# Kernel tuning notes

Measured on AMD Instinct MI355X. Metric: run time of the kernel, lower is better.

The kernel has to match this reference:

```python
import jax, jax.numpy as jnp
import numpy as np

NEG_BIG = -9.0e15  # matches torch zero_vec constant


def setup_inputs() -> dict:
    key = jax.random.key(0)
    k1, k2, k3, k4, k5 = jax.random.split(key, 5)
    B, N, D_IN, D_HID, D_OUT = 4, 4096, 128, 64, 128
    h = jax.random.normal(k1, (B, N, D_IN), dtype=jnp.float32)
    adj = jax.random.randint(k2, (N, N), 0, 2, dtype=jnp.int32)
    Ws = jax.random.normal(k3, (D_IN, D_HID), dtype=jnp.float32) * (1.414 / np.sqrt(D_IN))
    Wt = jax.random.normal(k4, (D_IN, D_HID), dtype=jnp.float32) * (1.414 / np.sqrt(D_IN))
    Wc = jax.random.normal(k5, (D_IN, D_OUT), dtype=jnp.float32) * np.sqrt(2.0 / D_IN)
    return {"h": h, "adj": adj, "Ws": Ws, "Wt": Wt, "Wc": Wc}


def reference(h, adj, Ws, Wt, Wc):
    # h: [B,N,D_in], adj: [N,N] broadcast over batch
    Whs = jnp.matmul(h, Ws)                     # [B,N,H]
    Wht = jnp.matmul(h, Wt)                     # [B,N,H]
    e = jnp.einsum('bnh,bmh->bnm', Whs, Wht)    # [B,N,N] dense scores
    z = jnp.where(adj > 0, e, NEG_BIG)          # adjacency mask
    alpha = jax.nn.softmax(z, axis=-1)          # [B,N,N]
    Whc = jnp.matmul(h, Wc)                     # [B,N,D_out]
    h_prime = jnp.matmul(alpha, Whc)            # [B,N,D_out]
    return h_prime
```

## Files before the change

kernel.cpp:

```cpp
#include <hip/hip_runtime.h>
#include <hip/hip_bf16.h>

#define NTOK 4096
#define BATCH 4
#define DIN 128
#define DHID 64
#define DOUT 128
#define NWRD (NTOK / 32)
#define NEG_BIG -9.0e15f
#define LOG2E 1.44269504088896340736f

typedef short short8 __attribute__((ext_vector_type(8)));
typedef float floatx4 __attribute__((ext_vector_type(4)));

static __device__ __forceinline__ unsigned short f2bf(float f) {
    unsigned int u = __builtin_bit_cast(unsigned int, f);
    u = (u + 0x7fffu + ((u >> 16) & 1u)) >> 16;
    return (unsigned short)u;
}
static __device__ __forceinline__ float bf2f(unsigned short s) {
    unsigned int u = ((unsigned int)s) << 16;
    return __builtin_bit_cast(float, u);
}
static __device__ __forceinline__ unsigned int pk2(float lo, float hi) {
    unsigned int r;
    asm("v_cvt_pk_bf16_f32 %0, %1, %2" : "=v"(r) : "v"(lo), "v"(hi));
    return r;
}

static __device__ __forceinline__ floatx4 mfma16(short8 a, short8 b, floatx4 c) {
    return __builtin_amdgcn_mfma_f32_16x16x32_bf16(a, b, c, 0, 0, 0);
}

__global__ __launch_bounds__(256) void pack_adj_kernel(const int* __restrict__ adj,
                                                       unsigned int* __restrict__ bits) {
    int w = blockIdx.x * 256 + threadIdx.x;
    const int4* p = reinterpret_cast<const int4*>(adj) + (size_t)w * 8;
    unsigned int m = 0;
#pragma unroll
    for (int i = 0; i < 8; ++i) {
        int4 v = p[i];
        m |= (v.x > 0 ? 1u : 0u) << (4 * i + 0);
        m |= (v.y > 0 ? 1u : 0u) << (4 * i + 1);
        m |= (v.z > 0 ? 1u : 0u) << (4 * i + 2);
        m |= (v.w > 0 ? 1u : 0u) << (4 * i + 3);
    }
    bits[w] = m;
}

__global__ __launch_bounds__(256) void conv_w_kernel(const float* __restrict__ Ws,
                                                     const float* __restrict__ Wt,
                                                     const float* __restrict__ Wc,
                                                     unsigned short* __restrict__ WT_hi,
                                                     unsigned short* __restrict__ WT_lo) {
    int idx = blockIdx.x * 256 + threadIdx.x;
    int k = idx >> 8, col = idx & 255;
    float w;
    if (col < 64) w = Ws[k * DHID + col] * LOG2E;
    else if (col < 128) w = Wt[k * DHID + (col - 64)];
    else w = Wc[k * DOUT + (col - 128)];
    unsigned short hi = f2bf(w);
    WT_hi[col * DIN + k] = hi;
    if (col < 128) WT_lo[col * DIN + k] = f2bf(w - bf2f(hi));
}

__global__ __launch_bounds__(256) void prep_kernel(const float* __restrict__ h,
                                                   const unsigned short* __restrict__ WT_hi,
                                                   const unsigned short* __restrict__ WT_lo,
                                                   unsigned short* __restrict__ Whs_hi,
                                                   unsigned short* __restrict__ Whs_lo,
                                                   unsigned short* __restrict__ Wht_hi,
                                                   unsigned short* __restrict__ Wht_lo,
                                                   unsigned short* __restrict__ WhcT) {
    int tid = threadIdx.x;
    int b = blockIdx.y;
    int w = tid >> 6, lane = tid & 63, lg = lane >> 4, lc = lane & 15;
    int n0 = blockIdx.x * 16;
    const float* hrow = h + (size_t)(b * NTOK + n0 + lc) * DIN;

    short8 ah[4], al[4];
#pragma unroll
    for (int ks = 0; ks < 4; ++ks) {
        float4 f0 = *reinterpret_cast<const float4*>(hrow + ks * 32 + lg * 8);
        float4 f1 = *reinterpret_cast<const float4*>(hrow + ks * 32 + lg * 8 + 4);
        float x[8] = {f0.x, f0.y, f0.z, f0.w, f1.x, f1.y, f1.z, f1.w};
        short8 hh, ll;
#pragma unroll
        for (int j = 0; j < 8; ++j) {
            unsigned short hb = f2bf(x[j]);
            hh[j] = (short)hb;
            ll[j] = (short)f2bf(x[j] - bf2f(hb));
        }
        ah[ks] = hh;
        al[ks] = ll;
    }

#pragma unroll
    for (int ci = 0; ci < 4; ++ci) {
        int ct = w * 4 + ci;
        int col = ct * 16 + lc;
        const unsigned short* bbase = WT_hi + (size_t)col * DIN;
        const unsigned short* lbase = WT_lo + (size_t)col * DIN;
        floatx4 acc = {0.f, 0.f, 0.f, 0.f};
#pragma unroll
        for (int ks = 0; ks < 4; ++ks) {
            short8 bh = *reinterpret_cast<const short8*>(bbase + ks * 32 + lg * 8);
            acc = mfma16(ah[ks], bh, acc);
            if (w < 2) {
                short8 bl = *reinterpret_cast<const short8*>(lbase + ks * 32 + lg * 8);
                acc = mfma16(ah[ks], bl, acc);
                acc = mfma16(al[ks], bh, acc);
            }
        }
        int nr = n0 + 4 * lg;
        if (w == 0) {
#pragma unroll
            for (int r = 0; r < 4; ++r) {
                float v = acc[r];
                unsigned short hb = f2bf(v);
                size_t o = (size_t)(b * NTOK + nr + r) * DHID + col;
                Whs_hi[o] = hb;
                Whs_lo[o] = f2bf(v - bf2f(hb));
            }
        } else if (w == 1) {
#pragma unroll
            for (int r = 0; r < 4; ++r) {
                float v = acc[r];
                unsigned short hb = f2bf(v);
                size_t o = (size_t)(b * NTOK + nr + r) * DHID + (col - 64);
                Wht_hi[o] = hb;
                Wht_lo[o] = f2bf(v - bf2f(hb));
            }
        } else {
            unsigned int p01 = (unsigned int)f2bf(acc[0]) | ((unsigned int)f2bf(acc[1]) << 16);
            unsigned int p23 = (unsigned int)f2bf(acc[2]) | ((unsigned int)f2bf(acc[3]) << 16);
            unsigned int* dst =
                reinterpret_cast<unsigned int*>(&WhcT[(size_t)(b * DOUT + col - 128) * NTOK + nr]);
            dst[0] = p01;
            dst[1] = p23;
        }
    }
}

template <int ITERS>
__global__ __launch_bounds__(256, 2) void attn_kernel(const unsigned short* __restrict__ Whs_hi,
                                                      const unsigned short* __restrict__ Whs_lo,
                                                      const unsigned short* __restrict__ Wht_hi,
                                                      const unsigned short* __restrict__ Wht_lo,
                                                      const unsigned short* __restrict__ WhcT,
                                                      const unsigned int* __restrict__ bits,
                                                      unsigned short* __restrict__ po,
                                                      float* __restrict__ pm,
                                                      float* __restrict__ pl) {
    __shared__ unsigned short Kh_lds[64][72];
    __shared__ unsigned short Kl_lds[64][72];
    __shared__ unsigned short V_lds[128][72];

    int tid = threadIdx.x;
    int b = blockIdx.y;
    int split = blockIdx.z;
    int kbase = split * (ITERS * 64);
    int lane = tid & 63, lg = lane >> 4, lc = lane & 15;
    int q0 = blockIdx.x * 128 + (tid >> 6) * 32;
    int nA = q0 + lc, nB = q0 + 16 + lc;

    const unsigned short* qAH = Whs_hi + (size_t)(b * NTOK + nA) * DHID;
    const unsigned short* qAL = Whs_lo + (size_t)(b * NTOK + nA) * DHID;
    const unsigned short* qBH = Whs_hi + (size_t)(b * NTOK + nB) * DHID;
    const unsigned short* qBL = Whs_lo + (size_t)(b * NTOK + nB) * DHID;
    short8 qAh0 = *reinterpret_cast<const short8*>(qAH + lg * 8);
    short8 qAh1 = *reinterpret_cast<const short8*>(qAH + 32 + lg * 8);
    short8 qAl0 = *reinterpret_cast<const short8*>(qAL + lg * 8);
    short8 qAl1 = *reinterpret_cast<const short8*>(qAL + 32 + lg * 8);
    short8 qBh0 = *reinterpret_cast<const short8*>(qBH + lg * 8);
    short8 qBh1 = *reinterpret_cast<const short8*>(qBH + 32 + lg * 8);
    short8 qBl0 = *reinterpret_cast<const short8*>(qBL + lg * 8);
    short8 qBl1 = *reinterpret_cast<const short8*>(qBL + 32 + lg * 8);

    floatx4 o0[8], o1[8];
#pragma unroll
    for (int dt = 0; dt < 8; ++dt) {
        o0[dt] = (floatx4){0.f, 0.f, 0.f, 0.f};
        o1[dt] = (floatx4){0.f, 0.f, 0.f, 0.f};
    }
    float mA = NEG_BIG, lA = 0.f, mB = NEG_BIG, lB = 0.f;

    int kkey = tid >> 2, koff = (tid & 3) * 16;
    int vd = tid >> 1, va = tid & 1;

    short8 krH0, krH1, krL0, krL1, vr0, vr1, vr2, vr3;
    unsigned int mwA0, mwA1, mwB0, mwB1;

    {
        int kb = kbase;
        const unsigned short* ksrcH = Wht_hi + (size_t)(b * NTOK + kb + kkey) * DHID + koff;
        const unsigned short* ksrcL = Wht_lo + (size_t)(b * NTOK + kb + kkey) * DHID + koff;
        krH0 = *reinterpret_cast<const short8*>(ksrcH);
        krH1 = *reinterpret_cast<const short8*>(ksrcH + 8);
        krL0 = *reinterpret_cast<const short8*>(ksrcL);
        krL1 = *reinterpret_cast<const short8*>(ksrcL + 8);
        const unsigned short* vsrc = WhcT + (size_t)(b * DOUT + vd) * NTOK + kb + va * 32;
        vr0 = *reinterpret_cast<const short8*>(vsrc);
        vr1 = *reinterpret_cast<const short8*>(vsrc + 8);
        vr2 = *reinterpret_cast<const short8*>(vsrc + 16);
        vr3 = *reinterpret_cast<const short8*>(vsrc + 24);
        mwA0 = bits[nA * NWRD + (kb >> 5)];
        mwA1 = bits[nA * NWRD + (kb >> 5) + 1];
        mwB0 = bits[nB * NWRD + (kb >> 5)];
        mwB1 = bits[nB * NWRD + (kb >> 5) + 1];
    }

    for (int it = 0; it < ITERS; ++it) {
        __syncthreads();
        *reinterpret_cast<short8*>(&Kh_lds[kkey][koff]) = krH0;
        *reinterpret_cast<short8*>(&Kh_lds[kkey][koff + 8]) = krH1;
        *reinterpret_cast<short8*>(&Kl_lds[kkey][koff]) = krL0;
        *reinterpret_cast<short8*>(&Kl_lds[kkey][koff + 8]) = krL1;
        {
            int sb = va * 32;
            short8 w00 = __builtin_shufflevector(vr0, vr2, 0, 1, 2, 3, 8, 9, 10, 11);
            short8 w01 = __builtin_shufflevector(vr0, vr2, 4, 5, 6, 7, 12, 13, 14, 15);
            short8 w10 = __builtin_shufflevector(vr1, vr3, 0, 1, 2, 3, 8, 9, 10, 11);
            short8 w11 = __builtin_shufflevector(vr1, vr3, 4, 5, 6, 7, 12, 13, 14, 15);
            *reinterpret_cast<short8*>(&V_lds[vd][sb]) = w00;
            *reinterpret_cast<short8*>(&V_lds[vd][sb + 8]) = w01;
            *reinterpret_cast<short8*>(&V_lds[vd][sb + 16]) = w10;
            *reinterpret_cast<short8*>(&V_lds[vd][sb + 24]) = w11;
        }
        __syncthreads();

        floatx4 s0[4], s1[4];
        __builtin_amdgcn_s_setprio(1);
#pragma unroll
        for (int kc = 0; kc < 4; ++kc) {
            short8 kh0 = *reinterpret_cast<const short8*>(&Kh_lds[kc * 16 + lc][lg * 8]);
            short8 kh1 = *reinterpret_cast<const short8*>(&Kh_lds[kc * 16 + lc][32 + lg * 8]);
            short8 kl0 = *reinterpret_cast<const short8*>(&Kl_lds[kc * 16 + lc][lg * 8]);
            short8 kl1 = *reinterpret_cast<const short8*>(&Kl_lds[kc * 16 + lc][32 + lg * 8]);
            floatx4 a0 = {0.f, 0.f, 0.f, 0.f};
            a0 = mfma16(kh0, qAh0, a0);
            a0 = mfma16(kh1, qAh1, a0);
            a0 = mfma16(kh0, qAl0, a0);
            a0 = mfma16(kh1, qAl1, a0);
            a0 = mfma16(kl0, qAh0, a0);
            a0 = mfma16(kl1, qAh1, a0);
            s0[kc] = a0;
            floatx4 a1 = {0.f, 0.f, 0.f, 0.f};
            a1 = mfma16(kh0, qBh0, a1);
            a1 = mfma16(kh1, qBh1, a1);
            a1 = mfma16(kh0, qBl0, a1);
            a1 = mfma16(kh1, qBl1, a1);
            a1 = mfma16(kl0, qBh0, a1);
            a1 = mfma16(kl1, qBh1, a1);
            s1[kc] = a1;
        }
        __builtin_amdgcn_s_setprio(0);

#pragma unroll
        for (int kc = 0; kc < 4; ++kc) {
            unsigned int wA = (kc & 2) ? mwA1 : mwA0;
            unsigned int wB = (kc & 2) ? mwB1 : mwB0;
#pragma unroll
            for (int r = 0; r < 4; ++r) {
                int bit = 16 * (kc & 1) + 4 * lg + r;
                if (!((wA >> bit) & 1u)) s0[kc][r] = NEG_BIG;
                if (!((wB >> bit) & 1u)) s1[kc][r] = NEG_BIG;
            }
        }

        if (it + 1 < ITERS) {
            int kb = kbase + (it + 1) * 64;
            const unsigned short* ksrcH = Wht_hi + (size_t)(b * NTOK + kb + kkey) * DHID + koff;
            const unsigned short* ksrcL = Wht_lo + (size_t)(b * NTOK + kb + kkey) * DHID + koff;
            krH0 = *reinterpret_cast<const short8*>(ksrcH);
            krH1 = *reinterpret_cast<const short8*>(ksrcH + 8);
            krL0 = *reinterpret_cast<const short8*>(ksrcL);
            krL1 = *reinterpret_cast<const short8*>(ksrcL + 8);
            const unsigned short* vsrc = WhcT + (size_t)(b * DOUT + vd) * NTOK + kb + va * 32;
            vr0 = *reinterpret_cast<const short8*>(vsrc);
            vr1 = *reinterpret_cast<const short8*>(vsrc + 8);
            vr2 = *reinterpret_cast<const short8*>(vsrc + 16);
            vr3 = *reinterpret_cast<const short8*>(vsrc + 24);
            mwA0 = bits[nA * NWRD + (kb >> 5)];
            mwA1 = bits[nA * NWRD + (kb >> 5) + 1];
            mwB0 = bits[nB * NWRD + (kb >> 5)];
            mwB1 = bits[nB * NWRD + (kb >> 5) + 1];
        }

        {
            float vm = s0[0][0];
#pragma unroll
            for (int kc = 0; kc < 4; ++kc)
#pragma unroll
                for (int r = 0; r < 4; ++r) vm = fmaxf(vm, s0[kc][r]);
            vm = fmaxf(vm, __shfl_xor(vm, 16));
            vm = fmaxf(vm, __shfl_xor(vm, 32));
            bool skip = __all(vm <= mA + 4.0f);
            float mn = skip ? mA : fmaxf(mA, vm);
            float rs = 0.f;
#pragma unroll
            for (int kc = 0; kc < 4; ++kc)
#pragma unroll
                for (int r = 0; r < 4; ++r) {
                    float p = exp2f(s0[kc][r] - mn);
                    s0[kc][r] = p;
                    rs += p;
                }
            rs += __shfl_xor(rs, 16);
            rs += __shfl_xor(rs, 32);
            if (!skip) {
                float sc = exp2f(mA - mn);
                lA = lA * sc + rs;
                mA = mn;
                float sc4[4];
#pragma unroll
                for (int r = 0; r < 4; ++r) sc4[r] = __shfl(sc, (lane & 48) + 4 * lg + r);
#pragma unroll
                for (int dt = 0; dt < 8; ++dt)
#pragma unroll
                    for (int r = 0; r < 4; ++r) o0[dt][r] *= sc4[r];
            } else {
                lA += rs;
            }
        }
        {
            float vm = s1[0][0];
#pragma unroll
            for (int kc = 0; kc < 4; ++kc)
#pragma unroll
                for (int r = 0; r < 4; ++r) vm = fmaxf(vm, s1[kc][r]);
            vm = fmaxf(vm, __shfl_xor(vm, 16));
            vm = fmaxf(vm, __shfl_xor(vm, 32));
            bool skip = __all(vm <= mB + 4.0f);
            float mn = skip ? mB : fmaxf(mB, vm);
            float rs = 0.f;
#pragma unroll
            for (int kc = 0; kc < 4; ++kc)
#pragma unroll
                for (int r = 0; r < 4; ++r) {
                    float p = exp2f(s1[kc][r] - mn);
                    s1[kc][r] = p;
                    rs += p;
                }
            rs += __shfl_xor(rs, 16);
            rs += __shfl_xor(rs, 32);
            if (!skip) {
                float sc = exp2f(mB - mn);
                lB = lB * sc + rs;
                mB = mn;
                float sc4[4];
#pragma unroll
                for (int r = 0; r < 4; ++r) sc4[r] = __shfl(sc, (lane & 48) + 4 * lg + r);
#pragma unroll
                for (int dt = 0; dt < 8; ++dt)
#pragma unroll
                    for (int r = 0; r < 4; ++r) o1[dt][r] *= sc4[r];
            } else {
                lB += rs;
            }
        }

        unsigned int pw[8];
        pw[0] = pk2(s0[0][0], s0[0][1]); pw[1] = pk2(s0[0][2], s0[0][3]);
        pw[2] = pk2(s0[1][0], s0[1][1]); pw[3] = pk2(s0[1][2], s0[1][3]);
        pw[4] = pk2(s0[2][0], s0[2][1]); pw[5] = pk2(s0[2][2], s0[2][3]);
        pw[6] = pk2(s0[3][0], s0[3][1]); pw[7] = pk2(s0[3][2], s0[3][3]);
        short8 paA0 = __builtin_bit_cast(short8, *reinterpret_cast<uint4*>(&pw[0]));
        short8 paA1 = __builtin_bit_cast(short8, *reinterpret_cast<uint4*>(&pw[4]));
        pw[0] = pk2(s1[0][0], s1[0][1]); pw[1] = pk2(s1[0][2], s1[0][3]);
        pw[2] = pk2(s1[1][0], s1[1][1]); pw[3] = pk2(s1[1][2], s1[1][3]);
        pw[4] = pk2(s1[2][0], s1[2][1]); pw[5] = pk2(s1[2][2], s1[2][3]);
        pw[6] = pk2(s1[3][0], s1[3][1]); pw[7] = pk2(s1[3][2], s1[3][3]);
        short8 paB0 = __builtin_bit_cast(short8, *reinterpret_cast<uint4*>(&pw[0]));
        short8 paB1 = __builtin_bit_cast(short8, *reinterpret_cast<uint4*>(&pw[4]));

        __builtin_amdgcn_s_setprio(1);
#pragma unroll
        for (int dt = 0; dt < 8; ++dt) {
            short8 vf0 = *reinterpret_cast<const short8*>(&V_lds[dt * 16 + lc][lg * 8]);
            o0[dt] = mfma16(paA0, vf0, o0[dt]);
            o1[dt] = mfma16(paB0, vf0, o1[dt]);
        }
#pragma unroll
        for (int dt = 0; dt < 8; ++dt) {
            short8 vf1 = *reinterpret_cast<const short8*>(&V_lds[dt * 16 + lc][32 + lg * 8]);
            o0[dt] = mfma16(paA1, vf1, o0[dt]);
            o1[dt] = mfma16(paB1, vf1, o1[dt]);
        }
        __builtin_amdgcn_s_setprio(0);
    }

    {
        float m4[4], l4[4];
#pragma unroll
        for (int r = 0; r < 4; ++r) {
            int src = (lane & 48) + 4 * lg + r;
            m4[r] = __shfl(mA, src);
            l4[r] = __shfl(lA, src);
        }
#pragma unroll
        for (int r = 0; r < 4; ++r) {
            size_t row = (size_t)(split * BATCH + b) * NTOK + q0 + 4 * lg + r;
            unsigned short* prow = po + row * DOUT;
#pragma unroll
            for (int dt = 0; dt < 8; ++dt) prow[dt * 16 + lc] = f2bf(o0[dt][r]);
            if (lc == 0) {
                pm[row] = m4[r];
                pl[row] = l4[r];
            }
        }
#pragma unroll
        for (int r = 0; r < 4; ++r) {
            int src = (lane & 48) + 4 * lg + r;
            m4[r] = __shfl(mB, src);
            l4[r] = __shfl(lB, src);
        }
#pragma unroll
        for (int r = 0; r < 4; ++r) {
            size_t row = (size_t)(split * BATCH + b) * NTOK + q0 + 16 + 4 * lg + r;
            unsigned short* prow = po + row * DOUT;
#pragma unroll
            for (int dt = 0; dt < 8; ++dt) prow[dt * 16 + lc] = f2bf(o1[dt][r]);
            if (lc == 0) {
                pm[row] = m4[r];
                pl[row] = l4[r];
            }
        }
    }
}

template <int NSPLIT>
__global__ __launch_bounds__(256) void merge_kernel(const unsigned short* __restrict__ po,
                                                    const float* __restrict__ pm,
                                                    const float* __restrict__ pl,
                                                    float* __restrict__ out) {
    int idx = blockIdx.x * 256 + threadIdx.x;
    int d = idx & (DOUT - 1);
    size_t bn = (size_t)(idx >> 7);
    const size_t BN = (size_t)BATCH * NTOK;

    float ms[NSPLIT];
#pragma unroll
    for (int s = 0; s < NSPLIT; ++s) ms[s] = pm[s * BN + bn];
    float M = ms[0];
#pragma unroll
    for (int s = 1; s < NSPLIT; ++s) M = fmaxf(M, ms[s]);
    float L = 0.f, acc = 0.f;
#pragma unroll
    for (int s = 0; s < NSPLIT; ++s) {
        float e = exp2f(ms[s] - M);
        L += pl[s * BN + bn] * e;
        acc += bf2f(po[(s * BN + bn) * DOUT + d]) * e;
    }
    out[idx] = acc / L;
}

extern "C" void kernel_launch(void* const* d_in, const int* in_sizes, int n_in,
                              void* d_out, int out_size, void* d_ws, size_t ws_size,
                              hipStream_t stream) {
    const float* h   = (const float*)d_in[0];
    const int*   adj = (const int*)d_in[1];
    const float* Ws  = (const float*)d_in[2];
    const float* Wt  = (const float*)d_in[3];
    const float* Wc  = (const float*)d_in[4];
    float* out = (float*)d_out;

    size_t nq = (size_t)BATCH * NTOK * DHID;
    unsigned short* Whs_hi = (unsigned short*)d_ws;
    unsigned short* Whs_lo = Whs_hi + nq;
    unsigned short* Wht_hi = Whs_lo + nq;
    unsigned short* Wht_lo = Wht_hi + nq;
    unsigned short* WhcT   = Wht_lo + nq;
    unsigned int*   bits   = (unsigned int*)(WhcT + (size_t)BATCH * DOUT * NTOK);
    unsigned short* WT_hi  = (unsigned short*)(bits + (size_t)NTOK * NWRD);
    unsigned short* WT_lo  = WT_hi + 256 * DIN;
    unsigned short* po     = WT_lo + 128 * DIN;
    const size_t BASE = (size_t)((char*)po - (char*)d_ws);

    size_t need8 = BASE + 8 * ((size_t)BATCH * NTOK * DOUT * 2 + (size_t)BATCH * NTOK * 8);
    int use8 = (ws_size >= need8) ? 1 : 0;
    int nsplit = use8 ? 8 : 4;

    float* pm = (float*)(po + (size_t)nsplit * BATCH * NTOK * DOUT);
    float* pl = pm + (size_t)nsplit * BATCH * NTOK;

    pack_adj_kernel<<<dim3(NTOK * NWRD / 256), dim3(256), 0, stream>>>(adj, bits);
    conv_w_kernel<<<dim3(128), dim3(256), 0, stream>>>(Ws, Wt, Wc, WT_hi, WT_lo);
    prep_kernel<<<dim3(NTOK / 16, BATCH), dim3(256), 0, stream>>>(
        h, WT_hi, WT_lo, Whs_hi, Whs_lo, Wht_hi, Wht_lo, WhcT);
    if (use8) {
        attn_kernel<8><<<dim3(NTOK / 128, BATCH, 8), dim3(256), 0, stream>>>(
            Whs_hi, Whs_lo, Wht_hi, Wht_lo, WhcT, bits, po, pm, pl);
        merge_kernel<8><<<dim3(BATCH * NTOK * DOUT / 256), dim3(256), 0, stream>>>(po, pm, pl, out);
    } else {
        attn_kernel<16><<<dim3(NTOK / 128, BATCH, 4), dim3(256), 0, stream>>>(
            Whs_hi, Whs_lo, Wht_hi, Wht_lo, WhcT, bits, po, pm, pl);
        merge_kernel<4><<<dim3(BATCH * NTOK * DOUT / 256), dim3(256), 0, stream>>>(po, pm, pl, out);
    }
}
```

Before: 200.0 us.

## Double-buffer K/V tiles in LDS, pre-permute V layout, fix split to 4

The attention kernel now keeps two LDS buffers for the K (hi/lo) and V tiles. The next tile is written to the idle buffer after compute, and global loads are issued two iterations ahead, which removes one barrier per iteration. The V shuffle is moved into the prep kernel by storing WhcT in a pre-permuted column order, so the kernel writes registers straight to LDS. The split count is fixed at 4 instead of picking 8 when workspace allows. LDS use doubles, which may limit occupancy, and fewer splits give fewer blocks.

```diff
diff --git a/kernel.cpp b/kernel.cpp
--- a/kernel.cpp
+++ b/kernel.cpp
@@ -7,6 +7,8 @@
 #define DHID 64
 #define DOUT 128
 #define NWRD (NTOK / 32)
+#define SPLIT 4
+#define ITERS (NTOK / SPLIT / 64)
 #define NEG_BIG -9.0e15f
 #define LOG2E 1.44269504088896340736f
 
@@ -132,17 +134,17 @@
                 Wht_lo[o] = f2bf(v - bf2f(hb));
             }
         } else {
+            int pcol = (nr & ~31) | ((nr & 8) << 1) | ((nr & 4) << 1) | ((nr & 16) >> 2);
             unsigned int p01 = (unsigned int)f2bf(acc[0]) | ((unsigned int)f2bf(acc[1]) << 16);
             unsigned int p23 = (unsigned int)f2bf(acc[2]) | ((unsigned int)f2bf(acc[3]) << 16);
             unsigned int* dst =
-                reinterpret_cast<unsigned int*>(&WhcT[(size_t)(b * DOUT + col - 128) * NTOK + nr]);
+                reinterpret_cast<unsigned int*>(&WhcT[(size_t)(b * DOUT + col - 128) * NTOK + pcol]);
             dst[0] = p01;
             dst[1] = p23;
         }
     }
 }
 
-template <int ITERS>
 __global__ __launch_bounds__(256, 2) void attn_kernel(const unsigned short* __restrict__ Whs_hi,
                                                       const unsigned short* __restrict__ Whs_lo,
                                                       const unsigned short* __restrict__ Wht_hi,
@@ -152,9 +154,9 @@
                                                       unsigned short* __restrict__ po,
                                                       float* __restrict__ pm,
                                                       float* __restrict__ pl) {
-    __shared__ unsigned short Kh_lds[64][72];
-    __shared__ unsigned short Kl_lds[64][72];
-    __shared__ unsigned short V_lds[128][72];
+    __shared__ unsigned short Kh_lds[2][64][72];
+    __shared__ unsigned short Kl_lds[2][64][72];
+    __shared__ unsigned short V_lds[2][128][72];
 
     int tid = threadIdx.x;
     int b = blockIdx.y;
@@ -208,35 +210,40 @@
         mwA1 = bits[nA * NWRD + (kb >> 5) + 1];
         mwB0 = bits[nB * NWRD + (kb >> 5)];
         mwB1 = bits[nB * NWRD + (kb >> 5) + 1];
+        *reinterpret_cast<short8*>(&Kh_lds[0][kkey][koff]) = krH0;
+        *reinterpret_cast<short8*>(&Kh_lds[0][kkey][koff + 8]) = krH1;
+        *reinterpret_cast<short8*>(&Kl_lds[0][kkey][koff]) = krL0;
+        *reinterpret_cast<short8*>(&Kl_lds[0][kkey][koff + 8]) = krL1;
+        *reinterpret_cast<short8*>(&V_lds[0][vd][va * 32]) = vr0;
+        *reinterpret_cast<short8*>(&V_lds[0][vd][va * 32 + 8]) = vr1;
+        *reinterpret_cast<short8*>(&V_lds[0][vd][va * 32 + 16]) = vr2;
+        *reinterpret_cast<short8*>(&V_lds[0][vd][va * 32 + 24]) = vr3;
+        int kb1 = kbase + 64;
+        const unsigned short* ksrcH1 = Wht_hi + (size_t)(b * NTOK + kb1 + kkey) * DHID + koff;
+        const unsigned short* ksrcL1 = Wht_lo + (size_t)(b * NTOK + kb1 + kkey) * DHID + koff;
+        krH0 = *reinterpret_cast<const short8*>(ksrcH1);
+        krH1 = *reinterpret_cast<const short8*>(ksrcH1 + 8);
+        krL0 = *reinterpret_cast<const short8*>(ksrcL1);
+        krL1 = *reinterpret_cast<const short8*>(ksrcL1 + 8);
+        const unsigned short* vsrc1 = WhcT + (size_t)(b * DOUT + vd) * NTOK + kb1 + va * 32;
+        vr0 = *reinterpret_cast<const short8*>(vsrc1);
+        vr1 = *reinterpret_cast<const short8*>(vsrc1 + 8);
+        vr2 = *reinterpret_cast<const short8*>(vsrc1 + 16);
+        vr3 = *reinterpret_cast<const short8*>(vsrc1 + 24);
     }
 
     for (int it = 0; it < ITERS; ++it) {
-        __syncthreads();
-        *reinterpret_cast<short8*>(&Kh_lds[kkey][koff]) = krH0;
-        *reinterpret_cast<short8*>(&Kh_lds[kkey][koff + 8]) = krH1;
-        *reinterpret_cast<short8*>(&Kl_lds[kkey][koff]) = krL0;
-        *reinterpret_cast<short8*>(&Kl_lds[kkey][koff + 8]) = krL1;
-        {
-            int sb = va * 32;
-            short8 w00 = __builtin_shufflevector(vr0, vr2, 0, 1, 2, 3, 8, 9, 10, 11);
-            short8 w01 = __builtin_shufflevector(vr0, vr2, 4, 5, 6, 7, 12, 13, 14, 15);
-            short8 w10 = __builtin_shufflevector(vr1, vr3, 0, 1, 2, 3, 8, 9, 10, 11);
-            short8 w11 = __builtin_shufflevector(vr1, vr3, 4, 5, 6, 7, 12, 13, 14, 15);
-            *reinterpret_cast<short8*>(&V_lds[vd][sb]) = w00;
-            *reinterpret_cast<short8*>(&V_lds[vd][sb + 8]) = w01;
-            *reinterpret_cast<short8*>(&V_lds[vd][sb + 16]) = w10;
-            *reinterpret_cast<short8*>(&V_lds[vd][sb + 24]) = w11;
-        }
+        const int cur = it & 1, nxt = cur ^ 1;
         __syncthreads();
 
         floatx4 s0[4], s1[4];
         __builtin_amdgcn_s_setprio(1);
 #pragma unroll
         for (int kc = 0; kc < 4; ++kc) {
-            short8 kh0 = *reinterpret_cast<const short8*>(&Kh_lds[kc * 16 + lc][lg * 8]);
-            short8 kh1 = *reinterpret_cast<const short8*>(&Kh_lds[kc * 16 + lc][32 + lg * 8]);
-            short8 kl0 = *reinterpret_cast<const short8*>(&Kl_lds[kc * 16 + lc][lg * 8]);
-            short8 kl1 = *reinterpret_cast<const short8*>(&Kl_lds[kc * 16 + lc][32 + lg * 8]);
+            short8 kh0 = *reinterpret_cast<const short8*>(&Kh_lds[cur][kc * 16 + lc][lg * 8]);
+            short8 kh1 = *reinterpret_cast<const short8*>(&Kh_lds[cur][kc * 16 + lc][32 + lg * 8]);
+            short8 kl0 = *reinterpret_cast<const short8*>(&Kl_lds[cur][kc * 16 + lc][lg * 8]);
+            short8 kl1 = *reinterpret_cast<const short8*>(&Kl_lds[cur][kc * 16 + lc][32 + lg * 8]);
             floatx4 a0 = {0.f, 0.f, 0.f, 0.f};
             a0 = mfma16(kh0, qAh0, a0);
             a0 = mfma16(kh1, qAh1, a0);
@@ -269,7 +276,17 @@
         }
 
         if (it + 1 < ITERS) {
-            int kb = kbase + (it + 1) * 64;
+            *reinterpret_cast<short8*>(&Kh_lds[nxt][kkey][koff]) = krH0;
+            *reinterpret_cast<short8*>(&Kh_lds[nxt][kkey][koff + 8]) = krH1;
+            *reinterpret_cast<short8*>(&Kl_lds[nxt][kkey][koff]) = krL0;
+            *reinterpret_cast<short8*>(&Kl_lds[nxt][kkey][koff + 8]) = krL1;
+            *reinterpret_cast<short8*>(&V_lds[nxt][vd][va * 32]) = vr0;
+            *reinterpret_cast<short8*>(&V_lds[nxt][vd][va * 32 + 8]) = vr1;
+            *reinterpret_cast<short8*>(&V_lds[nxt][vd][va * 32 + 16]) = vr2;
+            *reinterpret_cast<short8*>(&V_lds[nxt][vd][va * 32 + 24]) = vr3;
+        }
+        if (it + 2 < ITERS) {
+            int kb = kbase + (it + 2) * 64;
             const unsigned short* ksrcH = Wht_hi + (size_t)(b * NTOK + kb + kkey) * DHID + koff;
             const unsigned short* ksrcL = Wht_lo + (size_t)(b * NTOK + kb + kkey) * DHID + koff;
             krH0 = *reinterpret_cast<const short8*>(ksrcH);
@@ -281,6 +298,9 @@
             vr1 = *reinterpret_cast<const short8*>(vsrc + 8);
             vr2 = *reinterpret_cast<const short8*>(vsrc + 16);
             vr3 = *reinterpret_cast<const short8*>(vsrc + 24);
+        }
+        if (it + 1 < ITERS) {
+            int kb = kbase + (it + 1) * 64;
             mwA0 = bits[nA * NWRD + (kb >> 5)];
             mwA1 = bits[nA * NWRD + (kb >> 5) + 1];
             mwB0 = bits[nB * NWRD + (kb >> 5)];
@@ -377,13 +397,13 @@
         __builtin_amdgcn_s_setprio(1);
 #pragma unroll
         for (int dt = 0; dt < 8; ++dt) {
-            short8 vf0 = *reinterpret_cast<const short8*>(&V_lds[dt * 16 + lc][lg * 8]);
+            short8 vf0 = *reinterpret_cast<const short8*>(&V_lds[cur][dt * 16 + lc][lg * 8]);
             o0[dt] = mfma16(paA0, vf0, o0[dt]);
             o1[dt] = mfma16(paB0, vf0, o1[dt]);
         }
 #pragma unroll
         for (int dt = 0; dt < 8; ++dt) {
-            short8 vf1 = *reinterpret_cast<const short8*>(&V_lds[dt * 16 + lc][32 + lg * 8]);
+            short8 vf1 = *reinterpret_cast<const short8*>(&V_lds[cur][dt * 16 + lc][32 + lg * 8]);
             o0[dt] = mfma16(paA1, vf1, o0[dt]);
             o1[dt] = mfma16(paB1, vf1, o1[dt]);
         }
@@ -429,7 +449,6 @@
     }
 }
 
-template <int NSPLIT>
 __global__ __launch_bounds__(256) void merge_kernel(const unsigned short* __restrict__ po,
                                                     const float* __restrict__ pm,
                                                     const float* __restrict__ pl,
@@ -439,15 +458,15 @@
     size_t bn = (size_t)(idx >> 7);
     const size_t BN = (size_t)BATCH * NTOK;
 
-    float ms[NSPLIT];
-#pragma unroll
-    for (int s = 0; s < NSPLIT; ++s) ms[s] = pm[s * BN + bn];
+    float ms[SPLIT];
+#pragma unroll
+    for (int s = 0; s < SPLIT; ++s) ms[s] = pm[s * BN + bn];
     float M = ms[0];
 #pragma unroll
-    for (int s = 1; s < NSPLIT; ++s) M = fmaxf(M, ms[s]);
+    for (int s = 1; s < SPLIT; ++s) M = fmaxf(M, ms[s]);
     float L = 0.f, acc = 0.f;
 #pragma unroll
-    for (int s = 0; s < NSPLIT; ++s) {
+    for (int s = 0; s < SPLIT; ++s) {
         float e = exp2f(ms[s] - M);
         L += pl[s * BN + bn] * e;
         acc += bf2f(po[(s * BN + bn) * DOUT + d]) * e;
@@ -475,26 +494,14 @@
     unsigned short* WT_hi  = (unsigned short*)(bits + (size_t)NTOK * NWRD);
     unsigned short* WT_lo  = WT_hi + 256 * DIN;
     unsigned short* po     = WT_lo + 128 * DIN;
-    const size_t BASE = (size_t)((char*)po - (char*)d_ws);
-
-    size_t need8 = BASE + 8 * ((size_t)BATCH * NTOK * DOUT * 2 + (size_t)BATCH * NTOK * 8);
-    int use8 = (ws_size >= need8) ? 1 : 0;
-    int nsplit = use8 ? 8 : 4;
-
-    float* pm = (float*)(po + (size_t)nsplit * BATCH * NTOK * DOUT);
-    float* pl = pm + (size_t)nsplit * BATCH * NTOK;
+    float*          pm     = (float*)(po + (size_t)SPLIT * BATCH * NTOK * DOUT);
+    float*          pl     = pm + (size_t)SPLIT * BATCH * NTOK;
 
     pack_adj_kernel<<<dim3(NTOK * NWRD / 256), dim3(256), 0, stream>>>(adj, bits);
     conv_w_kernel<<<dim3(128), dim3(256), 0, stream>>>(Ws, Wt, Wc, WT_hi, WT_lo);
     prep_kernel<<<dim3(NTOK / 16, BATCH), dim3(256), 0, stream>>>(
         h, WT_hi, WT_lo, Whs_hi, Whs_lo, Wht_hi, Wht_lo, WhcT);
-    if (use8) {
-        attn_kernel<8><<<dim3(NTOK / 128, BATCH, 8), dim3(256), 0, stream>>>(
-            Whs_hi, Whs_lo, Wht_hi, Wht_lo, WhcT, bits, po, pm, pl);
-        merge_kernel<8><<<dim3(BATCH * NTOK * DOUT / 256), dim3(256), 0, stream>>>(po, pm, pl, out);
-    } else {
-        attn_kernel<16><<<dim3(NTOK / 128, BATCH, 4), dim3(256), 0, stream>>>(
-            Whs_hi, Whs_lo, Wht_hi, Wht_lo, WhcT, bits, po, pm, pl);
-        merge_kernel<4><<<dim3(BATCH * NTOK * DOUT / 256), dim3(256), 0, stream>>>(po, pm, pl, out);
-    }
-}
+    attn_kernel<<<dim3(NTOK / 128, BATCH, SPLIT), dim3(256), 0, stream>>>(
+        Whs_hi, Whs_lo, Wht_hi, Wht_lo, WhcT, bits, po, pm, pl);
+    merge_kernel<<<dim3(BATCH * NTOK * DOUT / 256), dim3(256), 0, stream>>>(po, pm, pl, out);
+}
```

After: 193.6 us. 3.2% less time.
